# Optimization experiments

Measured on AMD Instinct MI355X. Metric: run time of the kernel, lower is better.

## Reference

```python
import jax, jax.numpy as jnp
import numpy as np

E = 512      # embed_dim
H = 8        # num_heads
D = E // H   # head_dim


def setup_inputs() -> dict:
    key = jax.random.key(0)
    ks = jax.random.split(key, 10)
    T, S, B = 2048, 2048, 4
    inp = {}
    inp["query_r"] = jax.random.normal(ks[0], (T, B, E), jnp.float32)
    inp["query_i"] = jax.random.normal(ks[1], (T, B, E), jnp.float32)
    inp["key_r"]   = jax.random.normal(ks[2], (S, B, E), jnp.float32)
    inp["key_i"]   = jax.random.normal(ks[3], (S, B, E), jnp.float32)
    inp["value_r"] = jax.random.normal(ks[4], (S, B, E), jnp.float32)
    inp["value_i"] = jax.random.normal(ks[5], (S, B, E), jnp.float32)
    # xavier-ish scale for complex weights (split real/imag)
    w_scale = 1.0 / np.sqrt(2.0 * E)
    inp["in_w_r"]  = jax.random.normal(ks[6], (3 * E, E), jnp.float32) * w_scale
    inp["in_w_i"]  = jax.random.normal(ks[7], (3 * E, E), jnp.float32) * w_scale
    inp["in_b_r"]  = jnp.zeros((3 * E,), jnp.float32)
    inp["in_b_i"]  = jnp.zeros((3 * E,), jnp.float32)
    inp["out_w_r"] = jax.random.normal(ks[8], (E, E), jnp.float32) * w_scale
    inp["out_w_i"] = jax.random.normal(ks[9], (E, E), jnp.float32) * w_scale
    inp["out_b_r"] = jnp.zeros((E,), jnp.float32)
    inp["out_b_i"] = jnp.zeros((E,), jnp.float32)
    return inp


def _clinear(xr, xi, wr, wi, br, bi):
    # complex linear: (xr + i xi) @ (wr + i wi)^T + (br + i bi)
    yr = xr @ wr.T - xi @ wi.T + br
    yi = xr @ wi.T + xi @ wr.T + bi
    return yr, yi


def reference(query_r, query_i, key_r, key_i, value_r, value_i,
              in_w_r, in_w_i, in_b_r, in_b_i,
              out_w_r, out_w_i, out_b_r, out_b_i):
    T, B, _ = query_r.shape
    S = key_r.shape[0]
    # in-projection (packed q/k/v rows of in_proj_weight)
    qr, qi = _clinear(query_r, query_i, in_w_r[:E], in_w_i[:E], in_b_r[:E], in_b_i[:E])
    kr, ki = _clinear(key_r, key_i, in_w_r[E:2*E], in_w_i[E:2*E], in_b_r[E:2*E], in_b_i[E:2*E])
    vr, vi = _clinear(value_r, value_i, in_w_r[2*E:], in_w_i[2*E:], in_b_r[2*E:], in_b_i[2*E:])
    # split heads: (T,B,E) -> (T,B,H,D)
    qr = qr.reshape(T, B, H, D); qi = qi.reshape(T, B, H, D)
    kr = kr.reshape(S, B, H, D); ki = ki.reshape(S, B, H, D)
    vr = vr.reshape(S, B, H, D); vi = vi.reshape(S, B, H, D)
    scale = 1.0 / np.sqrt(D).astype(np.float32)
    # Re[Q K^H] = Qr.Kr + Qi.Ki  (conjugate transpose cancels imag cross terms)
    scores = (jnp.einsum('tbhd,sbhd->bhts', qr, kr)
              + jnp.einsum('tbhd,sbhd->bhts', qi, ki)) * scale
    p = jax.nn.softmax(scores, axis=-1)          # (B,H,T,S) real
    # complex AV with real attention weights
    or_ = jnp.einsum('bhts,sbhd->tbhd', p, vr).reshape(T, B, E)
    oi_ = jnp.einsum('bhts,sbhd->tbhd', p, vi).reshape(T, B, E)
    # out-projection (complex linear)
    out_r, out_i = _clinear(or_, oi_, out_w_r, out_w_i, out_b_r, out_b_i)
    attn_weights = p.mean(axis=1)                # averaged over heads: (B,T,S)
    return out_r, out_i, attn_weights
```

## Files before the change

kernel.cpp:

```cpp
#include <hip/hip_runtime.h>


typedef _Float16 half8 __attribute__((ext_vector_type(8)));
typedef _Float16 half2v __attribute__((ext_vector_type(2)));
typedef float f32x4 __attribute__((ext_vector_type(4)));
typedef float f32x2 __attribute__((ext_vector_type(2)));
typedef unsigned uint2v __attribute__((ext_vector_type(2)));
typedef unsigned uint4v __attribute__((ext_vector_type(4)));

__device__ __forceinline__ f32x4 mfma16(half8 a, half8 b, f32x4 c) {
  return __builtin_amdgcn_mfma_f32_16x16x32_f16(a, b, c, 0, 0, 0);
}

__device__ __forceinline__ half8 cvt8(f32x4 a, f32x4 b) {
  half8 h;
  h[0] = (_Float16)a[0]; h[1] = (_Float16)a[1]; h[2] = (_Float16)a[2]; h[3] = (_Float16)a[3];
  h[4] = (_Float16)b[0]; h[5] = (_Float16)b[1]; h[6] = (_Float16)b[2]; h[7] = (_Float16)b[3];
  return h;
}

__device__ __forceinline__ half8 neg8(half8 a) {
  half8 r;
#pragma unroll
  for (int i = 0; i < 8; i++) r[i] = -a[i];
  return r;
}

__device__ __forceinline__ unsigned pkrtz(float a, float b) {
  return __builtin_bit_cast(unsigned, __builtin_amdgcn_cvt_pkrtz(a, b));
}

__device__ __forceinline__ float fexp2(float x) { return __builtin_amdgcn_exp2f(x); }

__device__ __forceinline__ void gload16(const void* g, void* l) {
  __builtin_amdgcn_global_load_lds((const __attribute__((address_space(1))) void*)g,
                                   (__attribute__((address_space(3))) void*)l, 16, 0, 0);
}

__global__ __launch_bounds__(256) void cvt_weights_kernel(
    const float* __restrict__ iwr, const float* __restrict__ iwi,
    const float* __restrict__ owr, const float* __restrict__ owi,
    _Float16* __restrict__ dst) {
  const int i = blockIdx.x * 256 + threadIdx.x;
  const float* src;
  long so, doff;
  if (i < 98304)       { src = iwr; so = (long)i * 8;            doff = so; }
  else if (i < 196608) { src = iwi; so = (long)(i - 98304) * 8;  doff = 786432 + so; }
  else if (i < 229376) { src = owr; so = (long)(i - 196608) * 8; doff = 1572864 + so; }
  else                 { src = owi; so = (long)(i - 229376) * 8; doff = 1835008 + so; }
  f32x4 a = *(const f32x4*)(src + so);
  f32x4 b = *(const f32x4*)(src + so + 4);
  *(half8*)(dst + doff) = cvt8(a, b);
}

__global__ __launch_bounds__(256, 2) void inproj_kernel(
    const float* __restrict__ xqr, const float* __restrict__ xqi,
    const float* __restrict__ xkr, const float* __restrict__ xki,
    const float* __restrict__ xvr, const float* __restrict__ xvi,
    const _Float16* __restrict__ wr, const _Float16* __restrict__ wi,
    const float* __restrict__ br_, const float* __restrict__ bi_,
    _Float16* __restrict__ qp, _Float16* __restrict__ kp,
    _Float16* __restrict__ vp) {
  __shared__ float As_r[4096], As_i[4096];
  __shared__ _Float16 Bs_r[4096], Bs_i[4096];
  const int proj = blockIdx.z;
  const float* xr = (proj == 0) ? xqr : (proj == 1) ? xkr : xvr;
  const float* xi = (proj == 0) ? xqi : (proj == 1) ? xki : xvi;
  const int lane = threadIdx.x & 63, wave = threadIdx.x >> 6;
  const int c = lane & 15, g = lane >> 4;
  const int wrow = (wave >> 1) * 64, wcol = (wave & 1) * 64;
  const int m0 = blockIdx.x * 128, n0 = blockIdx.y * 128;

  const int acol = ((lane & 7) ^ (lane >> 3)) * 4;
  const int bcol = ((lane & 3) ^ ((lane >> 3) & 3)) * 8;
  const int sa = (c & 7) << 2;
  const int sb = ((c >> 1) & 3) << 3;

  f32x4 accR[4][4] = {};
  f32x4 accI[4][4] = {};

#pragma unroll 1
  for (int kk = 0; kk < 512; kk += 32) {
#pragma unroll
    for (int q = 0; q < 4; q++) {
      const int grp = wave * 4 + q;
      const int arow = grp * 8 + (lane >> 3);
      const long go = (long)(m0 + arow) * 512 + kk + acol;
      gload16(xr + go, &As_r[grp * 256]);
      gload16(xi + go, &As_i[grp * 256]);
    }
#pragma unroll
    for (int q = 0; q < 2; q++) {
      const int grp = wave * 2 + q;
      const int brow = grp * 16 + (lane >> 2);
      const long go = (long)(proj * 512 + n0 + brow) * 512 + kk + bcol;
      gload16(wr + go, &Bs_r[grp * 512]);
      gload16(wi + go, &Bs_i[grp * 512]);
    }
    __syncthreads();
    half8 a_r[4], a_i[4], a_ni[4];
#pragma unroll
    for (int mt = 0; mt < 4; mt++) {
      const int arow = wrow + mt * 16 + c;
      f32x4 lo = *(const f32x4*)&As_r[arow * 32 + ((g * 8) ^ sa)];
      f32x4 hi = *(const f32x4*)&As_r[arow * 32 + ((g * 8 + 4) ^ sa)];
      a_r[mt] = cvt8(lo, hi);
      lo = *(const f32x4*)&As_i[arow * 32 + ((g * 8) ^ sa)];
      hi = *(const f32x4*)&As_i[arow * 32 + ((g * 8 + 4) ^ sa)];
      a_i[mt] = cvt8(lo, hi);
      a_ni[mt] = neg8(a_i[mt]);
    }
#pragma unroll
    for (int nt = 0; nt < 4; nt++) {
      const int brow = wcol + nt * 16 + c;
      const half8 bR = *(const half8*)&Bs_r[brow * 32 + ((g * 8) ^ sb)];
      const half8 bI = *(const half8*)&Bs_i[brow * 32 + ((g * 8) ^ sb)];
#pragma unroll
      for (int mt = 0; mt < 4; mt++) {
        accR[mt][nt] = mfma16(a_r[mt], bR, accR[mt][nt]);
        accR[mt][nt] = mfma16(a_ni[mt], bI, accR[mt][nt]);
        accI[mt][nt] = mfma16(a_r[mt], bI, accI[mt][nt]);
        accI[mt][nt] = mfma16(a_i[mt], bR, accI[mt][nt]);
      }
    }
    __syncthreads();
  }
#pragma unroll
  for (int nt = 0; nt < 4; nt++) {
    const int n = n0 + wcol + nt * 16 + c;
    const float vbr = br_[proj * 512 + n];
    const float vbi = bi_[proj * 512 + n];
    const int hh = n >> 6, dl = n & 63;
#pragma unroll
    for (int mt = 0; mt < 4; mt++)
#pragma unroll
      for (int r = 0; r < 4; r++) {
        const int m = m0 + wrow + mt * 16 + g * 4 + r;
        const float yr = accR[mt][nt][r] + vbr;
        const float yi = accI[mt][nt][r] + vbi;
        const int row = m >> 2, bb = m & 3;
        if (proj == 2) {
          const long o = ((long)((bb * 8 + hh) * 64 + (row >> 5)) << 12)
                       + ((long)(dl >> 4) << 10)
                       + ((((row >> 3) & 3) * 16 + (dl & 15)) * 8) + (row & 7);
          vp[o] = (_Float16)yr;
          vp[o + 512] = (_Float16)yi;
        } else {
          const long o = ((long)((bb * 8 + hh) * 128 + (row >> 4)) << 11)
                       + ((long)(dl >> 5) << 10)
                       + ((((dl >> 3) & 3) * 16 + (row & 15)) * 8) + (dl & 7);
          _Float16* dst = (proj == 0) ? qp : kp;
          dst[o] = (_Float16)yr;
          dst[o + 512] = (_Float16)yi;
        }
      }
  }
}

__device__ __forceinline__ void p1_load(half8 (&a)[8],
    const _Float16* kb, int s0) {
  const _Float16* p = kb + (long)(s0 >> 4) * 2048;
#pragma unroll
  for (int j = 0; j < 4; j++) {
    a[j]     = *(const half8*)(p + j * 512);
    a[4 + j] = *(const half8*)(p + 2048 + j * 512);
  }
}

__device__ __forceinline__ void p1_proc(const half8 (&a)[8], const half8 (&qf)[4],
                                        float& mrun, float& lrun) {
  const float SC2 = 0.18033688011112042f;
  f32x4 acc0 = {0.f, 0.f, 0.f, 0.f}, acc1 = {0.f, 0.f, 0.f, 0.f};
  acc0 = mfma16(a[0], qf[0], acc0);
  acc0 = mfma16(a[1], qf[1], acc0);
  acc0 = mfma16(a[2], qf[2], acc0);
  acc0 = mfma16(a[3], qf[3], acc0);
  acc1 = mfma16(a[4], qf[0], acc1);
  acc1 = mfma16(a[5], qf[1], acc1);
  acc1 = mfma16(a[6], qf[2], acc1);
  acc1 = mfma16(a[7], qf[3], acc1);
  float s2[8];
#pragma unroll
  for (int r = 0; r < 4; r++) { s2[r] = acc0[r] * SC2; s2[4 + r] = acc1[r] * SC2; }
  float tm = s2[0];
#pragma unroll
  for (int j = 1; j < 8; j++) tm = fmaxf(tm, s2[j]);
  const float nm = fmaxf(mrun, tm);
  float sum = 0.0f;
#pragma unroll
  for (int j = 0; j < 8; j++) sum += fexp2(s2[j] - nm);
  lrun = lrun * fexp2(mrun - nm) + sum;
  mrun = nm;
}

__global__ __launch_bounds__(256) void pass1_kernel(
    const _Float16* __restrict__ qp, const _Float16* __restrict__ kp,
    float* __restrict__ m_out, float* __restrict__ r_out) {
  const int lane = threadIdx.x & 63, wave = threadIdx.x >> 6;
  const int c = lane & 15;
  const int lin = blockIdx.x;
  const int h = lin & 7, b = (lin >> 3) & 3;
  const int t0 = (lin >> 5) * 64 + wave * 16;

  const _Float16* qb = qp + ((long)(b * 8 + h) * 128 + (t0 >> 4)) * 2048 + lane * 8;
  half8 qf[4];
#pragma unroll
  for (int j = 0; j < 4; j++) qf[j] = *(const half8*)(qb + j * 512);

  float mrun = -1e30f, lrun = 0.0f;
  const _Float16* kb = kp + (long)(b * 8 + h) * 262144 + lane * 8;

  half8 bufA[8], bufB[8];
  p1_load(bufA, kb, 0);
  p1_load(bufB, kb, 32);
#pragma unroll 1
  for (int s0 = 0; s0 < 2048; s0 += 64) {
    p1_proc(bufA, qf, mrun, lrun);
    p1_load(bufA, kb, (s0 + 64) & 2047);
    p1_proc(bufB, qf, mrun, lrun);
    p1_load(bufB, kb, (s0 + 96) & 2047);
  }
#pragma unroll
  for (int off = 16; off <= 32; off <<= 1) {
    const float mo = __shfl_xor(mrun, off, 64);
    const float lo = __shfl_xor(lrun, off, 64);
    const float nm = fmaxf(mrun, mo);
    lrun = lrun * fexp2(mrun - nm) + lo * fexp2(mo - nm);
    mrun = nm;
  }
  if (lane < 16) {
    const int idx = (b * 8 + h) * 2048 + t0 + c;
    m_out[idx] = mrun;
    r_out[idx] = 1.0f / lrun;
  }
}

__device__ __forceinline__ void load_kswap(half8 (&kf)[8],
    const _Float16* kb, int s) {
  const _Float16* p = kb + (long)(s >> 4) * 2048;
#pragma unroll
  for (int j = 0; j < 4; j++) {
    kf[j]     = *(const half8*)(p + j * 512);
    kf[4 + j] = *(const half8*)(p + 2048 + j * 512);
  }
}

__device__ __forceinline__ void load_vv(half8 (&vf)[8],
    const _Float16* vb, int s) {
  const _Float16* p = vb + (long)(s >> 5) * 4096;
#pragma unroll
  for (int t = 0; t < 8; t++) vf[t] = *(const half8*)(p + t * 512);
}

__device__ __forceinline__ void p2_step(
    int s0, _Float16* pbuf, half8 (&kf)[8], half8 (&vf)[8],
    const half8 (&qf)[8], float nm0, float r0, float nm1, float r1,
    f32x4 (&oacc)[2][4][2], float* attn_base,
    const _Float16* kb, const _Float16* vb,
    int c, int g, int h, int tid) {
  const float SC2 = 0.18033688011112042f;
  f32x4 sacc[2][2];
#pragma unroll
  for (int st = 0; st < 2; st++)
#pragma unroll
    for (int sq = 0; sq < 2; sq++) {
      f32x4 a = {0.f, 0.f, 0.f, 0.f};
      a = mfma16(kf[sq * 4 + 0], qf[st * 4 + 0], a);
      a = mfma16(kf[sq * 4 + 1], qf[st * 4 + 1], a);
      a = mfma16(kf[sq * 4 + 2], qf[st * 4 + 2], a);
      a = mfma16(kf[sq * 4 + 3], qf[st * 4 + 3], a);
      sacc[st][sq] = a;
    }
  const int sn = (s0 + 32) & 2047;
  load_kswap(kf, kb, sn);
  half8 pa0, pa1;
#pragma unroll
  for (int st = 0; st < 2; st++) {
    const float nm = st ? nm1 : nm0;
    const float rv = st ? r1 : r0;
    float p[8];
#pragma unroll
    for (int r = 0; r < 4; r++) {
      p[r]     = fexp2(fmaf(sacc[st][0][r], SC2, nm)) * rv;
      p[4 + r] = fexp2(fmaf(sacc[st][1][r], SC2, nm)) * rv;
    }
    const unsigned X0 = pkrtz(p[0], p[1]), X1 = pkrtz(p[2], p[3]);
    const unsigned Y0 = pkrtz(p[4], p[5]), Y1 = pkrtz(p[6], p[7]);
    const uint2v ab0 = __builtin_amdgcn_permlane32_swap(X0, Y0, false, false);
    const uint2v ab1 = __builtin_amdgcn_permlane32_swap(X1, Y1, false, false);
    const uint2v cd0 = __builtin_amdgcn_permlane16_swap(ab0[0], ab0[1], false, false);
    const uint2v cd1 = __builtin_amdgcn_permlane16_swap(ab1[0], ab1[1], false, false);
    uint4v u;
    u[0] = cd0[0]; u[1] = cd1[0]; u[2] = cd0[1]; u[3] = cd1[1];
    const half8 pav = __builtin_bit_cast(half8, u);
    if (st == 0) pa0 = pav; else pa1 = pav;
    *(half8*)(pbuf + (h * 32 + st * 16 + c) * 40 + g * 8) = pav;
  }
#pragma unroll
  for (int dt = 0; dt < 4; dt++) {
    oacc[0][dt][0] = mfma16(pa0, vf[dt * 2 + 0], oacc[0][dt][0]);
    oacc[0][dt][1] = mfma16(pa0, vf[dt * 2 + 1], oacc[0][dt][1]);
    oacc[1][dt][0] = mfma16(pa1, vf[dt * 2 + 0], oacc[1][dt][0]);
    oacc[1][dt][1] = mfma16(pa1, vf[dt * 2 + 1], oacc[1][dt][1]);
  }
  load_vv(vf, vb, sn);
  __syncthreads();
  {
    const _Float16* mp = pbuf + (tid >> 4) * 40 + (tid & 15) * 2;
    float a0 = 0.f, a1 = 0.f;
#pragma unroll
    for (int w = 0; w < 8; w++) {
      const half2v v = *(const half2v*)(mp + w * 1280);
      a0 += (float)v[0];
      a1 += (float)v[1];
    }
    f32x2 out2 = {a0 * 0.125f, a1 * 0.125f};
    *(f32x2*)(attn_base + s0) = out2;
  }
}

__global__ __launch_bounds__(512, 2) void pass2_kernel(
    const _Float16* __restrict__ qp, const _Float16* __restrict__ kp,
    const _Float16* __restrict__ vp,
    const float* __restrict__ m_in, const float* __restrict__ r_in,
    _Float16* __restrict__ orh, _Float16* __restrict__ oih,
    float* __restrict__ attn) {
  __shared__ _Float16 plds[2][8][32][40];
  const int tid = threadIdx.x;
  const int lane = tid & 63, h = tid >> 6;
  const int c = lane & 15, g = lane >> 4;
  const int lin = blockIdx.x;
  const int b = (lin & 7) >> 1;
  const int t0 = (((lin & 1) << 5) | (lin >> 3)) * 32;

  const _Float16* qb = qp + ((long)(b * 8 + h) * 128 + (t0 >> 4)) * 2048 + lane * 8;
  half8 qf[8];
#pragma unroll
  for (int st = 0; st < 2; st++)
#pragma unroll
    for (int j = 0; j < 4; j++)
      qf[st * 4 + j] = *(const half8*)(qb + st * 2048 + j * 512);

  const int midx = (b * 8 + h) * 2048 + t0 + c;
  const float nm0 = -m_in[midx],      rr0 = r_in[midx];
  const float nm1 = -m_in[midx + 16], rr1 = r_in[midx + 16];

  f32x4 oacc[2][4][2] = {};
  const _Float16* kb = kp + (long)(b * 8 + h) * 262144 + lane * 8;
  const _Float16* vb = vp + (long)(b * 8 + h) * 262144 + lane * 8;
  float* attn_base = attn + ((long)b * 2048 + t0 + (tid >> 4)) * 2048 + (tid & 15) * 2;
  _Float16* pb0 = &plds[0][0][0][0];
  _Float16* pb1 = &plds[1][0][0][0];

  half8 kf[8], vf[8];
  load_kswap(kf, kb, 0);
  load_vv(vf, vb, 0);

#pragma unroll 1
  for (int s0 = 0; s0 < 2048; s0 += 64) {
    p2_step(s0, pb0, kf, vf, qf, nm0, rr0, nm1, rr1, oacc, attn_base,
            kb, vb, c, g, h, tid);
    p2_step(s0 + 32, pb1, kf, vf, qf, nm0, rr0, nm1, rr1, oacc, attn_base,
            kb, vb, c, g, h, tid);
  }
#pragma unroll
  for (int st = 0; st < 2; st++)
#pragma unroll
    for (int dt = 0; dt < 4; dt++)
#pragma unroll
      for (int r = 0; r < 4; r++) {
        const int t = t0 + st * 16 + g * 4 + r;
        const long row = (long)(t * 4 + b) * 512 + h * 64 + dt * 16 + c;
        orh[row] = (_Float16)oacc[st][dt][0][r];
        oih[row] = (_Float16)oacc[st][dt][1][r];
      }
}

__global__ __launch_bounds__(256, 2) void outproj_kernel(
    const _Float16* __restrict__ xr, const _Float16* __restrict__ xi,
    const _Float16* __restrict__ wr, const _Float16* __restrict__ wi,
    const float* __restrict__ br_, const float* __restrict__ bi_,
    float* __restrict__ outr, float* __restrict__ outi) {
  __shared__ _Float16 As_r[4096], As_i[4096];
  __shared__ _Float16 Bs_r[4096], Bs_i[4096];
  const int lane = threadIdx.x & 63, wave = threadIdx.x >> 6;
  const int c = lane & 15, g = lane >> 4;
  const int wrow = (wave >> 1) * 64, wcol = (wave & 1) * 64;
  const int m0 = blockIdx.x * 128, n0 = blockIdx.y * 128;

  const int bcol = ((lane & 3) ^ ((lane >> 3) & 3)) * 8;
  const int sb = ((c >> 1) & 3) << 3;

  f32x4 accR[4][4] = {};
  f32x4 accI[4][4] = {};

#pragma unroll 1
  for (int kk = 0; kk < 512; kk += 32) {
#pragma unroll
    for (int q = 0; q < 2; q++) {
      const int grp = wave * 2 + q;
      const int row = grp * 16 + (lane >> 2);
      const long ga = (long)(m0 + row) * 512 + kk + bcol;
      const long gb = (long)(n0 + row) * 512 + kk + bcol;
      gload16(xr + ga, &As_r[grp * 512]);
      gload16(xi + ga, &As_i[grp * 512]);
      gload16(wr + gb, &Bs_r[grp * 512]);
      gload16(wi + gb, &Bs_i[grp * 512]);
    }
    __syncthreads();
    half8 a_r[4], a_i[4], a_ni[4];
#pragma unroll
    for (int mt = 0; mt < 4; mt++) {
      const int arow = wrow + mt * 16 + c;
      a_r[mt] = *(const half8*)&As_r[arow * 32 + ((g * 8) ^ sb)];
      a_i[mt] = *(const half8*)&As_i[arow * 32 + ((g * 8) ^ sb)];
      a_ni[mt] = neg8(a_i[mt]);
    }
#pragma unroll
    for (int nt = 0; nt < 4; nt++) {
      const int brow = wcol + nt * 16 + c;
      const half8 bR = *(const half8*)&Bs_r[brow * 32 + ((g * 8) ^ sb)];
      const half8 bI = *(const half8*)&Bs_i[brow * 32 + ((g * 8) ^ sb)];
#pragma unroll
      for (int mt = 0; mt < 4; mt++) {
        accR[mt][nt] = mfma16(a_r[mt], bR, accR[mt][nt]);
        accR[mt][nt] = mfma16(a_ni[mt], bI, accR[mt][nt]);
        accI[mt][nt] = mfma16(a_r[mt], bI, accI[mt][nt]);
        accI[mt][nt] = mfma16(a_i[mt], bR, accI[mt][nt]);
      }
    }
    __syncthreads();
  }
#pragma unroll
  for (int nt = 0; nt < 4; nt++) {
    const int n = n0 + wcol + nt * 16 + c;
    const float vbr = br_[n], vbi = bi_[n];
#pragma unroll
    for (int mt = 0; mt < 4; mt++)
#pragma unroll
      for (int r = 0; r < 4; r++) {
        const int m = m0 + wrow + mt * 16 + g * 4 + r;
        outr[(long)m * 512 + n] = accR[mt][nt][r] + vbr;
        outi[(long)m * 512 + n] = accI[mt][nt][r] + vbi;
      }
  }
}

extern "C" void kernel_launch(void* const* d_in, const int* in_sizes, int n_in,
                              void* d_out, int out_size, void* d_ws, size_t ws_size,
                              hipStream_t stream) {
  const float* query_r = (const float*)d_in[0];
  const float* query_i = (const float*)d_in[1];
  const float* key_r   = (const float*)d_in[2];
  const float* key_i   = (const float*)d_in[3];
  const float* value_r = (const float*)d_in[4];
  const float* value_i = (const float*)d_in[5];
  const float* in_w_r  = (const float*)d_in[6];
  const float* in_w_i  = (const float*)d_in[7];
  const float* in_b_r  = (const float*)d_in[8];
  const float* in_b_i  = (const float*)d_in[9];
  const float* out_w_r = (const float*)d_in[10];
  const float* out_w_i = (const float*)d_in[11];
  const float* out_b_r = (const float*)d_in[12];
  const float* out_b_i = (const float*)d_in[13];

  _Float16* ws = (_Float16*)d_ws;
  _Float16* w16_inr  = ws;
  _Float16* w16_ini  = ws + 786432;
  _Float16* w16_outr = ws + 1572864;
  _Float16* w16_outi = ws + 1835008;
  _Float16* Qp  = ws + 2097152;
  _Float16* Kp  = Qp + 8388608;
  _Float16* Vp  = Kp + 8388608;
  _Float16* orh = Vp + 8388608;
  _Float16* oih = orh + 4194304;
  float* m_arr = (float*)ws;
  float* r_arr = m_arr + 65536;

  float* outr = (float*)d_out;
  float* outi = outr + 4194304;
  float* attn = outr + 8388608;

  cvt_weights_kernel<<<1024, 256, 0, stream>>>(in_w_r, in_w_i, out_w_r, out_w_i, ws);

  inproj_kernel<<<dim3(64, 4, 3), 256, 0, stream>>>(
      query_r, query_i, key_r, key_i, value_r, value_i,
      w16_inr, w16_ini, in_b_r, in_b_i,
      Qp, Kp, Vp);

  pass1_kernel<<<1024, 256, 0, stream>>>(Qp, Kp, m_arr, r_arr);

  pass2_kernel<<<256, 512, 0, stream>>>(
      Qp, Kp, Vp, m_arr, r_arr, orh, oih, attn);

  outproj_kernel<<<dim3(64, 4), 256, 0, stream>>>(
      orh, oih, w16_outr, w16_outi, out_b_r, out_b_i, outr, outi);
}
```

Measured before the change: 303.8 us.

## Defer head-mean readback one step, fold softmax normaliser, prioritize MFMA waves

The head-averaged attention readback in pass2 now runs one sub-step behind the compute, using a four-slot LDS ring. This leaves one barrier per sub-step and lets the mean reads overlap the next tile's compute. Pass1 now writes a single log-sum-exp constant, so pass2 drops the per-element reciprocal multiply. The MFMA blocks are wrapped in s_setprio raises, and the head sum is accumulated in fp16 rather than fp32, which trades some precision on attn_weights and doubles LDS use.

```diff
diff --git a/kernel.cpp b/kernel.cpp
--- a/kernel.cpp
+++ b/kernel.cpp
@@ -171,6 +171,7 @@
                                         float& mrun, float& lrun) {
   const float SC2 = 0.18033688011112042f;
   f32x4 acc0 = {0.f, 0.f, 0.f, 0.f}, acc1 = {0.f, 0.f, 0.f, 0.f};
+  __builtin_amdgcn_s_setprio(1);
   acc0 = mfma16(a[0], qf[0], acc0);
   acc0 = mfma16(a[1], qf[1], acc0);
   acc0 = mfma16(a[2], qf[2], acc0);
@@ -179,6 +180,7 @@
   acc1 = mfma16(a[5], qf[1], acc1);
   acc1 = mfma16(a[6], qf[2], acc1);
   acc1 = mfma16(a[7], qf[3], acc1);
+  __builtin_amdgcn_s_setprio(0);
   float s2[8];
 #pragma unroll
   for (int r = 0; r < 4; r++) { s2[r] = acc0[r] * SC2; s2[4 + r] = acc1[r] * SC2; }
@@ -195,7 +197,7 @@
 
 __global__ __launch_bounds__(256) void pass1_kernel(
     const _Float16* __restrict__ qp, const _Float16* __restrict__ kp,
-    float* __restrict__ m_out, float* __restrict__ r_out) {
+    float* __restrict__ c_out) {
   const int lane = threadIdx.x & 63, wave = threadIdx.x >> 6;
   const int c = lane & 15;
   const int lin = blockIdx.x;
@@ -230,8 +232,7 @@
   }
   if (lane < 16) {
     const int idx = (b * 8 + h) * 2048 + t0 + c;
-    m_out[idx] = mrun;
-    r_out[idx] = 1.0f / lrun;
+    c_out[idx] = -(mrun + __log2f(lrun));
   }
 }
 
@@ -252,14 +253,15 @@
   for (int t = 0; t < 8; t++) vf[t] = *(const half8*)(p + t * 512);
 }
 
-__device__ __forceinline__ void p2_step(
-    int s0, _Float16* pbuf, half8 (&kf)[8], half8 (&vf)[8],
-    const half8 (&qf)[8], float nm0, float r0, float nm1, float r1,
-    f32x4 (&oacc)[2][4][2], float* attn_base,
+__device__ __forceinline__ void p2_compute(
+    int s0, _Float16* wbuf, half8 (&kf)[8], half8 (&vf)[8],
+    const half8 (&qf)[8], float c0, float c1,
+    f32x4 (&oacc)[2][4][2],
     const _Float16* kb, const _Float16* vb,
-    int c, int g, int h, int tid) {
+    int c, int g, int h) {
   const float SC2 = 0.18033688011112042f;
   f32x4 sacc[2][2];
+  __builtin_amdgcn_s_setprio(1);
 #pragma unroll
   for (int st = 0; st < 2; st++)
 #pragma unroll
@@ -271,18 +273,18 @@
       a = mfma16(kf[sq * 4 + 3], qf[st * 4 + 3], a);
       sacc[st][sq] = a;
     }
+  __builtin_amdgcn_s_setprio(0);
   const int sn = (s0 + 32) & 2047;
   load_kswap(kf, kb, sn);
   half8 pa0, pa1;
 #pragma unroll
   for (int st = 0; st < 2; st++) {
-    const float nm = st ? nm1 : nm0;
-    const float rv = st ? r1 : r0;
+    const float cc = st ? c1 : c0;
     float p[8];
 #pragma unroll
     for (int r = 0; r < 4; r++) {
-      p[r]     = fexp2(fmaf(sacc[st][0][r], SC2, nm)) * rv;
-      p[4 + r] = fexp2(fmaf(sacc[st][1][r], SC2, nm)) * rv;
+      p[r]     = fexp2(fmaf(sacc[st][0][r], SC2, cc));
+      p[4 + r] = fexp2(fmaf(sacc[st][1][r], SC2, cc));
     }
     const unsigned X0 = pkrtz(p[0], p[1]), X1 = pkrtz(p[2], p[3]);
     const unsigned Y0 = pkrtz(p[4], p[5]), Y1 = pkrtz(p[6], p[7]);
@@ -294,8 +296,9 @@
     u[0] = cd0[0]; u[1] = cd1[0]; u[2] = cd0[1]; u[3] = cd1[1];
     const half8 pav = __builtin_bit_cast(half8, u);
     if (st == 0) pa0 = pav; else pa1 = pav;
-    *(half8*)(pbuf + (h * 32 + st * 16 + c) * 40 + g * 8) = pav;
-  }
+    *(half8*)(wbuf + (h * 32 + st * 16 + c) * 40 + g * 8) = pav;
+  }
+  __builtin_amdgcn_s_setprio(1);
 #pragma unroll
   for (int dt = 0; dt < 4; dt++) {
     oacc[0][dt][0] = mfma16(pa0, vf[dt * 2 + 0], oacc[0][dt][0]);
@@ -303,29 +306,27 @@
     oacc[1][dt][0] = mfma16(pa1, vf[dt * 2 + 0], oacc[1][dt][0]);
     oacc[1][dt][1] = mfma16(pa1, vf[dt * 2 + 1], oacc[1][dt][1]);
   }
+  __builtin_amdgcn_s_setprio(0);
   load_vv(vf, vb, sn);
-  __syncthreads();
-  {
-    const _Float16* mp = pbuf + (tid >> 4) * 40 + (tid & 15) * 2;
-    float a0 = 0.f, a1 = 0.f;
-#pragma unroll
-    for (int w = 0; w < 8; w++) {
-      const half2v v = *(const half2v*)(mp + w * 1280);
-      a0 += (float)v[0];
-      a1 += (float)v[1];
-    }
-    f32x2 out2 = {a0 * 0.125f, a1 * 0.125f};
-    *(f32x2*)(attn_base + s0) = out2;
-  }
+}
+
+__device__ __forceinline__ void p2_meanread(
+    const _Float16* rbuf, int s_read, float* attn_base, int tid) {
+  const _Float16* mp = rbuf + (tid >> 4) * 40 + (tid & 15) * 2;
+  half2v s = *(const half2v*)(mp);
+#pragma unroll
+  for (int w = 1; w < 8; w++) s += *(const half2v*)(mp + w * 1280);
+  f32x2 out2 = {(float)s[0] * 0.125f, (float)s[1] * 0.125f};
+  *(f32x2*)(attn_base + s_read) = out2;
 }
 
 __global__ __launch_bounds__(512, 2) void pass2_kernel(
     const _Float16* __restrict__ qp, const _Float16* __restrict__ kp,
     const _Float16* __restrict__ vp,
-    const float* __restrict__ m_in, const float* __restrict__ r_in,
+    const float* __restrict__ c_in,
     _Float16* __restrict__ orh, _Float16* __restrict__ oih,
     float* __restrict__ attn) {
-  __shared__ _Float16 plds[2][8][32][40];
+  __shared__ _Float16 plds[4][8][32][40];
   const int tid = threadIdx.x;
   const int lane = tid & 63, h = tid >> 6;
   const int c = lane & 15, g = lane >> 4;
@@ -342,8 +343,8 @@
       qf[st * 4 + j] = *(const half8*)(qb + st * 2048 + j * 512);
 
   const int midx = (b * 8 + h) * 2048 + t0 + c;
-  const float nm0 = -m_in[midx],      rr0 = r_in[midx];
-  const float nm1 = -m_in[midx + 16], rr1 = r_in[midx + 16];
+  const float c0 = c_in[midx];
+  const float c1 = c_in[midx + 16];
 
   f32x4 oacc[2][4][2] = {};
   const _Float16* kb = kp + (long)(b * 8 + h) * 262144 + lane * 8;
@@ -351,18 +352,30 @@
   float* attn_base = attn + ((long)b * 2048 + t0 + (tid >> 4)) * 2048 + (tid & 15) * 2;
   _Float16* pb0 = &plds[0][0][0][0];
   _Float16* pb1 = &plds[1][0][0][0];
+  _Float16* pb2 = &plds[2][0][0][0];
+  _Float16* pb3 = &plds[3][0][0][0];
 
   half8 kf[8], vf[8];
   load_kswap(kf, kb, 0);
   load_vv(vf, vb, 0);
 
 #pragma unroll 1
-  for (int s0 = 0; s0 < 2048; s0 += 64) {
-    p2_step(s0, pb0, kf, vf, qf, nm0, rr0, nm1, rr1, oacc, attn_base,
-            kb, vb, c, g, h, tid);
-    p2_step(s0 + 32, pb1, kf, vf, qf, nm0, rr0, nm1, rr1, oacc, attn_base,
-            kb, vb, c, g, h, tid);
-  }
+  for (int s0 = 0; s0 < 2048; s0 += 128) {
+    p2_compute(s0, pb0, kf, vf, qf, c0, c1, oacc, kb, vb, c, g, h);
+    __syncthreads();
+    if (s0 >= 32) p2_meanread(pb3, s0 - 32, attn_base, tid);
+    p2_compute(s0 + 32, pb1, kf, vf, qf, c0, c1, oacc, kb, vb, c, g, h);
+    __syncthreads();
+    p2_meanread(pb0, s0, attn_base, tid);
+    p2_compute(s0 + 64, pb2, kf, vf, qf, c0, c1, oacc, kb, vb, c, g, h);
+    __syncthreads();
+    p2_meanread(pb1, s0 + 32, attn_base, tid);
+    p2_compute(s0 + 96, pb3, kf, vf, qf, c0, c1, oacc, kb, vb, c, g, h);
+    __syncthreads();
+    p2_meanread(pb2, s0 + 64, attn_base, tid);
+  }
+  p2_meanread(pb3, 2016, attn_base, tid);
+
 #pragma unroll
   for (int st = 0; st < 2; st++)
 #pragma unroll
@@ -474,8 +487,7 @@
   _Float16* Vp  = Kp + 8388608;
   _Float16* orh = Vp + 8388608;
   _Float16* oih = orh + 4194304;
-  float* m_arr = (float*)ws;
-  float* r_arr = m_arr + 65536;
+  float* c_arr = (float*)ws;
 
   float* outr = (float*)d_out;
   float* outi = outr + 4194304;
@@ -488,10 +500,10 @@
       w16_inr, w16_ini, in_b_r, in_b_i,
       Qp, Kp, Vp);
 
-  pass1_kernel<<<1024, 256, 0, stream>>>(Qp, Kp, m_arr, r_arr);
+  pass1_kernel<<<1024, 256, 0, stream>>>(Qp, Kp, c_arr);
 
   pass2_kernel<<<256, 512, 0, stream>>>(
-      Qp, Kp, Vp, m_arr, r_arr, orh, oih, attn);
+      Qp, Kp, Vp, c_arr, orh, oih, attn);
 
   outproj_kernel<<<dim3(64, 4), 256, 0, stream>>>(
       orh, oih, w16_outr, w16_outi, out_b_r, out_b_i, outr, outi);
```

Result: faster. 284.0 us (-6.5%).
